# Kernel tuning notes

Measured on AMD Instinct MI355X. Metric: run time of the kernel, lower is better.

The kernel has to match this reference:

```python
import jax, jax.numpy as jnp
import numpy as np

jax.config.update("jax_enable_x64", True)

H = 16            # bits per coordinate
TP = 8            # number of coordinate trees
C = 4
DIV = 1
K = C * H // DIV  # 64 random masks per flipped bit
N = 2 ** H        # 65536, lookup table size / coord magnitude bound
M = 2 * H * K + 1 # 2049 connection candidates per token
B, T1, T2 = 4, 16, 32


def _lookup_table():
    # (floor(log2(x+1)) + 1) / h for x in [0, n)
    x = jnp.arange(N, dtype=jnp.float32)
    return (jnp.floor(jnp.log2(x + 1.0)) + 1.0) / H


def _distance(c1, c2, norm, table):
    # sign product * (1 - s) * norm, s gathered by XOR of magnitudes
    sg = jnp.where(c1 >= 0, 1.0, -1.0) * jnp.where(c2 >= 0, 1.0, -1.0)
    s = table[jnp.abs(c1) ^ jnp.abs(c2)]
    return sg * (1.0 - s) * norm


def _connection(ori, rand_raw, perm):
    # ori: [Nt, TP] nonnegative ints; rand_raw: [Nt, H, K, TP]; perm: [M]
    bits = jnp.arange(H, dtype=jnp.int64)
    flip_masks = (jnp.int64(1) << bits)[None, :, None]            # [1,H,1]
    flipped = ori[:, None, :] ^ flip_masks                         # [Nt,H,TP]
    upper = (jnp.int64(1) << bits)                                 # 2^j per level
    masks = rand_raw % upper[None, :, None, None]                  # [Nt,H,K,TP]
    result = (flipped[:, :, None, :] ^ masks).reshape(ori.shape[0], H * K, TP)
    loc = jnp.concatenate([result, ori[:, None, :], -result], axis=1)  # [Nt,M,TP]
    return loc[:, perm, :]


def setup_inputs() -> dict:
    key = jax.random.key(0)
    k1, k2, k3, k4, k5 = jax.random.split(key, 5)
    sta_loc = jax.random.randint(k1, (B, T1, TP), 1 - N, N, dtype=jnp.int64)
    pos_loc = jax.random.randint(k2, (B, T2, TP), 1 - N, N, dtype=jnp.int64)
    val_n = jax.random.uniform(k3, (B, T1, T2), dtype=jnp.float32)
    rand_raw = jax.random.randint(k4, (B * T1, H, K, TP), 0, N, dtype=jnp.int64)
    perm = jax.random.permutation(k5, M).astype(jnp.int64)
    return {"sta_loc": sta_loc, "pos_loc": pos_loc, "val_n": val_n,
            "rand_raw": rand_raw, "perm": perm}


def reference(sta_loc, pos_loc, val_n, rand_raw, perm):
    table = _lookup_table()
    # dis_sta_pos: [B,T1,T2,TP]
    dis_sta_pos = _distance(sta_loc[:, :, None, :], pos_loc[:, None, :, :],
                            val_n[..., None], table)
    # connection candidates from |sta_loc|: [B,T1,M,TP]
    cnc_loc = _connection(jnp.abs(sta_loc).reshape(-1, TP), rand_raw, perm)
    cnc_loc = cnc_loc.reshape(B, T1, M, TP)
    # dis_cnc_pos: [B,T1,T2,M,TP]
    dis_cnc_pos = _distance(cnc_loc[:, :, None, :, :], pos_loc[:, None, :, None, :],
                            val_n[..., None, None], table)
    dis_sum = dis_sta_pos.sum(axis=-1)  # [B,T1,T2]
    # ct_val: leave-one-tree-out swap of the candidate coordinate
    ct_val = (dis_sum[:, :, :, None, None] - dis_sta_pos[:, :, :, None, :]
              + dis_cnc_pos) / TP
    return ct_val
```

## Files before the change

### kernel.cpp

```cpp
#include <hip/hip_runtime.h>
#include <hip/hip_bf16.h>

#define BB 4
#define T1 16
#define T2 32
#define TPn 8
#define Hh 16
#define Kk 64
#define Mm 2049
#define NT2B 2

typedef float  floatx4 __attribute__((ext_vector_type(4)));
typedef int    intx4   __attribute__((ext_vector_type(4)));


__device__ __forceinline__ float omss16(int x) {
    int c = __clz(x + 1) - 16;
    if (x == 8191 || x == 32767) c += 1;
    return (float)c;
}

__global__ __launch_bounds__(256)
void critigraph_kernel(const int* __restrict__ sta_loc,
                       const int* __restrict__ pos_loc,
                       const float* __restrict__ val_n,
                       const int* __restrict__ rand_raw,
                       const int* __restrict__ perm,
                       float* __restrict__ out)
{
    const int bt  = blockIdx.x;
    const int b   = bt / T1;
    const int mc  = blockIdx.y;
    const int t2q = blockIdx.z;
    const int tid = threadIdx.x;

    __shared__ __align__(16) int   s_pabs[NT2B * TPn];
    __shared__ __align__(16) float s_vs8[NT2B * TPn];
    __shared__ __align__(16) float s_base8[NT2B * TPn];
    __shared__ float s_dis[NT2B * TPn];
    __shared__ float s_sum[NT2B];
    __shared__ int   s_ori[TPn];

    if (tid < TPn) {
        int sv = sta_loc[bt * TPn + tid];
        s_ori[tid] = sv < 0 ? -sv : sv;
    }
    if (tid < NT2B * TPn) {
        const int t2l = tid >> 3;
        const int tp  = tid & 7;
        const int t2  = t2q * NT2B + t2l;
        int pv = pos_loc[(b * T2 + t2) * TPn + tp];
        int pa = pv < 0 ? -pv : pv;
        float psgn = (pv >= 0) ? 1.0f : -1.0f;
        int sv = sta_loc[bt * TPn + tp];
        int sa = sv < 0 ? -sv : sv;
        float ssgn = (sv >= 0) ? 1.0f : -1.0f;
        float v = val_n[bt * T2 + t2];
        int x = sa ^ pa;
        s_dis[tid]  = ssgn * psgn * (omss16(x) * 0.0625f) * v;
        s_pabs[tid] = pa;
        s_vs8[tid]  = psgn * v * 0.125f;
    }
    __syncthreads();
    if (tid < NT2B) {
        const float* d = &s_dis[tid * TPn];
        float acc = 0.0f;
        #pragma unroll
        for (int tp = 0; tp < TPn; ++tp) acc += d[tp];
        s_sum[tid] = acc;
    }
    __syncthreads();
    if (tid < NT2B * TPn) {
        s_base8[tid] = (s_sum[tid >> 3] - s_dis[tid]) * 0.125f;
    }
    __syncthreads();

    const int q4 = (tid & 1) * 4;

    {
        const int m = mc * 128 + (tid >> 1);
        int   a[4];
        float sg16[4];
        const int pm = perm[m];
        if (pm == Hh * Kk) {
            #pragma unroll
            for (int j = 0; j < 4; ++j) { a[j] = s_ori[q4 + j]; sg16[j] = 0.0625f; }
        } else {
            const int r   = (pm < Hh * Kk) ? pm : pm - (Hh * Kk + 1);
            const float ng = (pm < Hh * Kk) ? 0.0625f : -0.0625f;
            const int jj  = r >> 6;
            const int k   = r & 63;
            const int mb  = (1 << jj) - 1;
            const int flip = 1 << jj;
            const int* rr = rand_raw + ((bt * Hh + jj) * Kk + k) * TPn + q4;
            #pragma unroll
            for (int j = 0; j < 4; ++j) {
                int res = (s_ori[q4 + j] ^ flip) ^ (rr[j] & mb);
                a[j] = res;
                sg16[j] = (res == 0) ? 0.0625f : ng;
            }
        }

        float* op = out + ((long long)(bt * T2 + t2q * NT2B) * Mm + m) * TPn + q4;
        #pragma unroll
        for (int t2l = 0; t2l < NT2B; ++t2l) {
            const int idx = t2l * TPn + q4;
            const intx4   pv = *(const intx4*)&s_pabs[idx];
            const floatx4 vs = *(const floatx4*)&s_vs8[idx];
            const floatx4 bs = *(const floatx4*)&s_base8[idx];
            floatx4 o;
            o.x = fmaf(omss16(a[0] ^ pv.x) * sg16[0], vs.x, bs.x);
            o.y = fmaf(omss16(a[1] ^ pv.y) * sg16[1], vs.y, bs.y);
            o.z = fmaf(omss16(a[2] ^ pv.z) * sg16[2], vs.z, bs.z);
            o.w = fmaf(omss16(a[3] ^ pv.w) * sg16[3], vs.w, bs.w);
            *(floatx4*)(op + (long long)t2l * (Mm * TPn)) = o;
        }
    }

    if (mc == 0 && tid < 2) {
        const int m = 2048;
        int   a[4];
        float sg16[4];
        const int pm = perm[m];
        if (pm == Hh * Kk) {
            #pragma unroll
            for (int j = 0; j < 4; ++j) { a[j] = s_ori[q4 + j]; sg16[j] = 0.0625f; }
        } else {
            const int r   = (pm < Hh * Kk) ? pm : pm - (Hh * Kk + 1);
            const float ng = (pm < Hh * Kk) ? 0.0625f : -0.0625f;
            const int jj  = r >> 6;
            const int k   = r & 63;
            const int mb  = (1 << jj) - 1;
            const int flip = 1 << jj;
            const int* rr = rand_raw + ((bt * Hh + jj) * Kk + k) * TPn + q4;
            #pragma unroll
            for (int j = 0; j < 4; ++j) {
                int res = (s_ori[q4 + j] ^ flip) ^ (rr[j] & mb);
                a[j] = res;
                sg16[j] = (res == 0) ? 0.0625f : ng;
            }
        }

        float* op = out + ((long long)(bt * T2 + t2q * NT2B) * Mm + m) * TPn + q4;
        #pragma unroll
        for (int t2l = 0; t2l < NT2B; ++t2l) {
            const int idx = t2l * TPn + q4;
            const intx4   pv = *(const intx4*)&s_pabs[idx];
            const floatx4 vs = *(const floatx4*)&s_vs8[idx];
            const floatx4 bs = *(const floatx4*)&s_base8[idx];
            floatx4 o;
            o.x = fmaf(omss16(a[0] ^ pv.x) * sg16[0], vs.x, bs.x);
            o.y = fmaf(omss16(a[1] ^ pv.y) * sg16[1], vs.y, bs.y);
            o.z = fmaf(omss16(a[2] ^ pv.z) * sg16[2], vs.z, bs.z);
            o.w = fmaf(omss16(a[3] ^ pv.w) * sg16[3], vs.w, bs.w);
            *(floatx4*)(op + (long long)t2l * (Mm * TPn)) = o;
        }
    }
}

extern "C" void kernel_launch(void* const* d_in, const int* in_sizes, int n_in,
                              void* d_out, int out_size, void* d_ws, size_t ws_size,
                              hipStream_t stream) {
    const int*   sta_loc  = (const int*)d_in[0];
    const int*   pos_loc  = (const int*)d_in[1];
    const float* val_n    = (const float*)d_in[2];
    const int*   rand_raw = (const int*)d_in[3];
    const int*   perm     = (const int*)d_in[4];
    float* out = (float*)d_out;

    dim3 grid(BB * T1, 16, 16);
    critigraph_kernel<<<grid, 256, 0, stream>>>(sta_loc, pos_loc, val_n,
                                                rand_raw, perm, out);
}
```

Baseline: 31.09 us.

## Process four t2 per block, use wave shuffles for tree sums, drop shared ori

```diff
diff --git a/kernel.cpp b/kernel.cpp
--- a/kernel.cpp
+++ b/kernel.cpp
@@ -8,7 +8,7 @@
 #define Hh 16
 #define Kk 64
 #define Mm 2049
-#define NT2B 2
+#define NT2B 4
 
 typedef float  floatx4 __attribute__((ext_vector_type(4)));
 typedef int    intx4   __attribute__((ext_vector_type(4)));
@@ -29,7 +29,7 @@
                        float* __restrict__ out)
 {
     const int bt  = blockIdx.x;
-    const int b   = bt / T1;
+    const int b   = bt >> 4;
     const int mc  = blockIdx.y;
     const int t2q = blockIdx.z;
     const int tid = threadIdx.x;
@@ -37,14 +37,7 @@
     __shared__ __align__(16) int   s_pabs[NT2B * TPn];
     __shared__ __align__(16) float s_vs8[NT2B * TPn];
     __shared__ __align__(16) float s_base8[NT2B * TPn];
-    __shared__ float s_dis[NT2B * TPn];
-    __shared__ float s_sum[NT2B];
-    __shared__ int   s_ori[TPn];
 
-    if (tid < TPn) {
-        int sv = sta_loc[bt * TPn + tid];
-        s_ori[tid] = sv < 0 ? -sv : sv;
-    }
     if (tid < NT2B * TPn) {
         const int t2l = tid >> 3;
         const int tp  = tid & 7;
@@ -56,26 +49,25 @@
         int sa = sv < 0 ? -sv : sv;
         float ssgn = (sv >= 0) ? 1.0f : -1.0f;
         float v = val_n[bt * T2 + t2];
-        int x = sa ^ pa;
-        s_dis[tid]  = ssgn * psgn * (omss16(x) * 0.0625f) * v;
-        s_pabs[tid] = pa;
-        s_vs8[tid]  = psgn * v * 0.125f;
-    }
-    __syncthreads();
-    if (tid < NT2B) {
-        const float* d = &s_dis[tid * TPn];
-        float acc = 0.0f;
-        #pragma unroll
-        for (int tp = 0; tp < TPn; ++tp) acc += d[tp];
-        s_sum[tid] = acc;
-    }
-    __syncthreads();
-    if (tid < NT2B * TPn) {
-        s_base8[tid] = (s_sum[tid >> 3] - s_dis[tid]) * 0.125f;
+        float d = ssgn * psgn * (omss16(sa ^ pa) * 0.0625f) * v;
+        float acc = d;
+        acc += __shfl_xor(acc, 1);
+        acc += __shfl_xor(acc, 2);
+        acc += __shfl_xor(acc, 4);
+        s_pabs[tid]  = pa;
+        s_vs8[tid]   = psgn * v * 0.125f;
+        s_base8[tid] = (acc - d) * 0.125f;
     }
     __syncthreads();
 
     const int q4 = (tid & 1) * 4;
+
+    int ori_t[4];
+    #pragma unroll
+    for (int j = 0; j < 4; ++j) {
+        int sv = sta_loc[bt * TPn + q4 + j];
+        ori_t[j] = sv < 0 ? -sv : sv;
+    }
 
     {
         const int m = mc * 128 + (tid >> 1);
@@ -84,7 +76,7 @@
         const int pm = perm[m];
         if (pm == Hh * Kk) {
             #pragma unroll
-            for (int j = 0; j < 4; ++j) { a[j] = s_ori[q4 + j]; sg16[j] = 0.0625f; }
+            for (int j = 0; j < 4; ++j) { a[j] = ori_t[j]; sg16[j] = 0.0625f; }
         } else {
             const int r   = (pm < Hh * Kk) ? pm : pm - (Hh * Kk + 1);
             const float ng = (pm < Hh * Kk) ? 0.0625f : -0.0625f;
@@ -95,7 +87,7 @@
             const int* rr = rand_raw + ((bt * Hh + jj) * Kk + k) * TPn + q4;
             #pragma unroll
             for (int j = 0; j < 4; ++j) {
-                int res = (s_ori[q4 + j] ^ flip) ^ (rr[j] & mb);
+                int res = (ori_t[j] ^ flip) ^ (rr[j] & mb);
                 a[j] = res;
                 sg16[j] = (res == 0) ? 0.0625f : ng;
             }
@@ -124,7 +116,7 @@
         const int pm = perm[m];
         if (pm == Hh * Kk) {
             #pragma unroll
-            for (int j = 0; j < 4; ++j) { a[j] = s_ori[q4 + j]; sg16[j] = 0.0625f; }
+            for (int j = 0; j < 4; ++j) { a[j] = ori_t[j]; sg16[j] = 0.0625f; }
         } else {
             const int r   = (pm < Hh * Kk) ? pm : pm - (Hh * Kk + 1);
             const float ng = (pm < Hh * Kk) ? 0.0625f : -0.0625f;
@@ -135,7 +127,7 @@
             const int* rr = rand_raw + ((bt * Hh + jj) * Kk + k) * TPn + q4;
             #pragma unroll
             for (int j = 0; j < 4; ++j) {
-                int res = (s_ori[q4 + j] ^ flip) ^ (rr[j] & mb);
+                int res = (ori_t[j] ^ flip) ^ (rr[j] & mb);
                 a[j] = res;
                 sg16[j] = (res == 0) ? 0.0625f : ng;
             }
@@ -168,7 +160,7 @@
     const int*   perm     = (const int*)d_in[4];
     float* out = (float*)d_out;
 
-    dim3 grid(BB * T1, 16, 16);
+    dim3 grid(BB * T1, 16, 8);
     critigraph_kernel<<<grid, 256, 0, stream>>>(sta_loc, pos_loc, val_n,
                                                 rand_raw, perm, out);
 }
```

New measurement: 27.56 us (median of 2 runs). 11.4% less time.
